# Kernel optimization log

Measured on AMD Instinct MI355X. Metric: run time of the kernel, lower is better.

The kernel has to match this reference:

```python
import jax, jax.numpy as jnp
import numpy as np

M1 = M2 = M3 = 8  # truncated Hartley modes (min(modes, in_channels) in original)


def dht(x):
    # Discrete Hartley transform via 3D FFT over spatial axes: real - imag
    r = jnp.fft.fftn(x, axes=(2, 3, 4))
    return r.real - r.imag


def _mul(a, w):
    # 'bixyz,ioxyz->boxyz' mode-wise channel mixing
    return jnp.einsum('bixyz,ioxyz->boxyz', a, w)


def setup_inputs() -> dict:
    key = jax.random.key(0)
    ks = jax.random.split(key, 5)
    B, Ci, Co = 2, 64, 64
    S1 = S2 = S3 = 64
    scale = 1.0 / (Ci * Co)
    x = jax.random.normal(ks[0], (B, Ci, S1, S2, S3), dtype=jnp.float32)
    wshape = (Ci, Co, M1, M2, M3)
    w1 = scale * jax.random.uniform(ks[1], wshape, dtype=jnp.float32)
    w2 = scale * jax.random.uniform(ks[2], wshape, dtype=jnp.float32)
    w3 = scale * jax.random.uniform(ks[3], wshape, dtype=jnp.float32)
    w4 = scale * jax.random.uniform(ks[4], wshape, dtype=jnp.float32)
    return {"x": x, "w1": w1, "w2": w2, "w3": w3, "w4": w4}


def reference(x, w1, w2, w3, w4):
    b, ci, s1, s2, s3 = x.shape
    co = w1.shape[1]
    # Hartley transform of x ("cos part") and of fully flipped x ("sin part")
    xh = dht(x)
    xhf = dht(x[:, :, ::-1, ::-1, ::-1])

    out_ht = jnp.zeros((b, co, s1, s2, s3), dtype=x.dtype)
    out_ht = out_ht.at[:, :, :M1, :M2, :M3].set(_mul(xh[:, :, :M1, :M2, :M3], w1))
    out_ht = out_ht.at[:, :, -M1:, :M2, :M3].set(_mul(xh[:, :, -M1:, :M2, :M3], w2))
    out_ht = out_ht.at[:, :, :M1, -M2:, :M3].set(_mul(xh[:, :, :M1, -M2:, :M3], w3))
    out_ht = out_ht.at[:, :, -M1:, -M2:, :M3].set(_mul(xh[:, :, -M1:, -M2:, :M3], w4))
    # original zeroes out_ht[:, :, M1:, M2:, M3:] — already zero here since 2*modes <= size

    # inverse DHT = DHT / (D*M*N)
    x_rec = dht(out_ht) / (s1 * s2 * s3)

    # phase = angle(complex(cos_part, sin_part)) = atan2(sin, cos), only on corner block; 0 elsewhere
    phase_corner = jnp.arctan2(xhf[:, :, :M1, :M2, :M3], xh[:, :, :M1, :M2, :M3])
    cos_phase = jnp.ones((b, ci, s1, s2, s3), dtype=x.dtype)
    cos_phase = cos_phase.at[:, :, :M1, :M2, :M3].set(jnp.cos(phase_corner))
    return x_rec * cos_phase
```

## Files before the change

### kernel.cpp

```cpp
#include <hip/hip_runtime.h>
#include <math.h>

struct cf2 { float x, y; };
struct TW64 { float c[64], s[64]; };
struct CF2T { cf2 v[64]; };

constexpr double PI_D = 3.14159265358979323846264338327950288;

constexpr double tsin(double x){
  double x2 = x*x, r = x, t = x;
  t *= -x2/6.0;   r += t;
  t *= -x2/20.0;  r += t;
  t *= -x2/42.0;  r += t;
  t *= -x2/72.0;  r += t;
  t *= -x2/110.0; r += t;
  t *= -x2/156.0; r += t;
  t *= -x2/210.0; r += t;
  t *= -x2/272.0; r += t;
  return r;
}
constexpr double tcos(double x){
  double x2 = x*x, r = 1.0, t = 1.0;
  t *= -x2/2.0;   r += t;
  t *= -x2/12.0;  r += t;
  t *= -x2/30.0;  r += t;
  t *= -x2/56.0;  r += t;
  t *= -x2/90.0;  r += t;
  t *= -x2/132.0; r += t;
  t *= -x2/182.0; r += t;
  t *= -x2/240.0; r += t;
  return r;
}
constexpr double ang_cos(int j){
  int r = j & 15, q = (j >> 4) & 3;
  double a = PI_D/32.0 * r;
  double cc = tcos(a), ss = tsin(a);
  return q==0 ? cc : q==1 ? -ss : q==2 ? -cc : ss;
}
constexpr double ang_sin(int j){
  int r = j & 15, q = (j >> 4) & 3;
  double a = PI_D/32.0 * r;
  double cc = tcos(a), ss = tsin(a);
  return q==0 ? ss : q==1 ? cc : q==2 ? -ss : -cc;
}
constexpr TW64 make_tw(){
  TW64 t{};
  for (int j=0;j<64;j++){ t.c[j] = (float)ang_cos(j); t.s[j] = (float)ang_sin(j); }
  return t;
}
constexpr CF2T make_twi(){
  CF2T r{};
  for (int j=0;j<64;j++){ r.v[j].x = (float)ang_cos(j); r.v[j].y = (float)ang_sin(j); }
  return r;
}
constexpr CF2T make_pq(){
  CF2T r{};
  for (int j=0;j<64;j++){
    double c = ang_cos(j), s = ang_sin(j);
    r.v[j].x = (float)((c + s) / 262144.0);
    r.v[j].y = (float)((s - c) / 262144.0);
  }
  return r;
}

constexpr TW64 TWct = make_tw();
__constant__ CF2T TWIdev = make_twi();
__constant__ CF2T PQdev  = make_pq();

__global__ __launch_bounds__(256) void k_fwd(const float* __restrict__ x, float2* __restrict__ y2g){
  __shared__ float2 y1[8][4][65];
  __shared__ cf2 twl[64];
  int bid = blockIdx.x;
  int n1g = bid & 15, ci_b = bid >> 4;
  int t = threadIdx.x;
  if (t < 64) twl[t] = TWIdev.v[t];
  int n1l = t >> 6, n2 = t & 63;
  int n1 = n1g*4 + n1l;
  const float4* xrow = (const float4*)(x + (((size_t)(ci_b*64 + n1))*64 + n2)*64);
  float xr[64];
  #pragma unroll
  for (int i=0;i<16;i++){
    float4 v = xrow[i];
    xr[4*i]=v.x; xr[4*i+1]=v.y; xr[4*i+2]=v.z; xr[4*i+3]=v.w;
  }
  float yr[8], yi[8];
  #pragma unroll
  for (int k=0;k<8;k++){ yr[k]=0.f; yi[k]=0.f; }
  #pragma unroll
  for (int n3=0;n3<64;n3++){
    float xv = xr[n3];
    #pragma unroll
    for (int k=0;k<8;k++){
      yr[k] = fmaf(xv,  TWct.c[(k*n3)&63], yr[k]);
      yi[k] = fmaf(xv, -TWct.s[(k*n3)&63], yi[k]);
    }
  }
  #pragma unroll
  for (int k=0;k<8;k++) y1[k][n1l][n2] = make_float2(yr[k], yi[k]);
  __syncthreads();
  int w = t >> 6, lane = t & 63;
  int n1c = lane >> 4, k3c = (lane >> 1) & 7, half = lane & 1;
  #pragma unroll
  for (int kk=0;kk<4;kk++){
    int k2i = w*4 + kk;
    int k2 = k2i < 8 ? k2i : 48 + k2i;
    int idx = (k2 * (half*32)) & 63;
    float ar = 0.f, ai = 0.f;
    #pragma unroll 8
    for (int i=0;i<32;i++){
      cf2 tw = twl[idx];
      idx = (idx + k2) & 63;
      float2 y = y1[k3c][n1c][half*32 + i];
      ar = fmaf(y.x, tw.x, fmaf(y.y, tw.y, ar));
      ai = fmaf(y.y, tw.x, fmaf(-y.x, tw.y, ai));
    }
    ar += __shfl_xor(ar, 1, 64);
    ai += __shfl_xor(ai, 1, 64);
    if (half == 0){
      int n1w = n1g*4 + n1c;
      y2g[((size_t)(ci_b*64 + n1w)*16 + k2i)*8 + k3c] = make_float2(ar, ai);
    }
  }
}

template<int K1B>
__device__ __forceinline__ void k2_body(const float2 (*yl)[128], int kk, float* ar, float* ai){
  for (int n1=0;n1<64;n1++){
    float2 y = yl[n1][kk];
    #pragma unroll
    for (int j=0;j<8;j++){
      int k1i = K1B + 2*j;
      int k1 = k1i < 8 ? k1i : 48 + k1i;
      cf2 tw = TWIdev.v[(k1*n1)&63];
      ar[j] = fmaf(y.x, tw.x, fmaf(y.y, tw.y, ar[j]));
      ai[j] = fmaf(y.y, tw.x, fmaf(-y.x, tw.y, ai[j]));
    }
  }
}

__global__ __launch_bounds__(256) void k_fwd_n1(const float2* __restrict__ y2g,
                                                float* __restrict__ xh, float* __restrict__ cp){
  __shared__ float2 yl[64][128];
  int bc = blockIdx.x;
  int t = threadIdx.x;
  const float2* src = y2g + (size_t)bc * 8192;
  #pragma unroll
  for (int j=0;j<32;j++){
    int idx = t + j*256;
    yl[idx>>7][idx&127] = src[idx];
  }
  __syncthreads();
  int kk = t & 127;
  int k2i = kk >> 3, k3 = kk & 7;
  float ar[8], ai[8];
  #pragma unroll
  for (int j=0;j<8;j++){ ar[j]=0.f; ai[j]=0.f; }
  if (t < 128) k2_body<0>(yl, kk, ar, ai);
  else         k2_body<1>(yl, kk, ar, ai);
  int k1base = t >> 7;
  size_t xbase = (size_t)bc * 2048;
  #pragma unroll
  for (int j=0;j<8;j++){
    int k1i = k1base + 2*j;
    float vr = ar[j], vi = ai[j];
    float vxh = vr - vi;
    xh[xbase + k1i*128 + kk] = vxh;
    if (k1i < 8 && k2i < 8){
      int phi = (k1i + k2i + k3) & 63;
      cf2 tw = TWIdev.v[phi];
      float vxhf = vr*(tw.x - tw.y) + vi*(tw.x + tw.y);
      cp[(size_t)bc*512 + k1i*64 + k2i*8 + k3] = cosf(atan2f(vxhf, vxh));
    }
  }
}

__global__ __launch_bounds__(256) void k_mix(const float* __restrict__ xh,
    const float* __restrict__ w1, const float* __restrict__ w2,
    const float* __restrict__ w3, const float* __restrict__ w4,
    float* __restrict__ mh){
  __shared__ float xs[2][64][64];
  __shared__ float wsh[64][64];
  __shared__ float ps[2][128];
  int bid = blockIdx.x;
  int k1l = bid & 7, co = (bid >> 3) & 63, blk = bid >> 9;
  const float* w = (blk==0) ? w1 : (blk==1) ? w2 : (blk==2) ? w3 : w4;
  int k1i = k1l + ((blk & 1) << 3);
  int k2off = (blk & 2) ? 64 : 0;
  int t = threadIdx.x;
  #pragma unroll
  for (int j=0;j<16;j++){
    int idx = t + j*256;
    int ci = idx >> 6, kk = idx & 63;
    wsh[ci][kk] = w[(size_t)(ci*64 + co)*512 + k1l*64 + kk];
  }
  #pragma unroll
  for (int j=0;j<32;j++){
    int idx = t + j*256;
    int b = idx >> 12, ci = (idx >> 6) & 63, kk = idx & 63;
    xs[b][ci][kk] = xh[(size_t)((b*64 + ci)*16 + k1i)*128 + k2off + kk];
  }
  __syncthreads();
  int half = t >> 7, o = t & 127, b = o >> 6, kk = o & 63;
  float acc = 0.f;
  #pragma unroll 8
  for (int i=0;i<32;i++){
    int ci = half*32 + i;
    acc = fmaf(xs[b][ci][kk], wsh[ci][kk], acc);
  }
  ps[half][o] = acc;
  __syncthreads();
  if (t < 128){
    int b2 = t >> 6, kk2 = t & 63;
    mh[(size_t)((b2*64 + co)*16 + k1i)*128 + k2off + kk2] = ps[0][t] + ps[1][t];
  }
}

__global__ __launch_bounds__(256) void k_inv(const float* __restrict__ mh,
                                             const float* __restrict__ cp,
                                             float* __restrict__ out){
  __shared__ float ml[2048];
  __shared__ float2 z1[16][8];
  __shared__ float2 z2[64][8];
  __shared__ cf2 twl[64];
  __shared__ cf2 pql[64];
  int bid = blockIdx.x;
  int n1 = bid & 63, bc = bid >> 6;
  int t = threadIdx.x;
  if (t < 64){ twl[t] = TWIdev.v[t]; pql[t] = PQdev.v[t]; }
  const float* src = mh + (size_t)bc * 2048;
  #pragma unroll
  for (int j=0;j<8;j++) ml[t + j*256] = src[t + j*256];
  __syncthreads();
  if (t < 128){
    float zr = 0.f, zi = 0.f;
    #pragma unroll
    for (int k1i=0;k1i<16;k1i++){
      int k1 = k1i < 8 ? k1i : 48 + k1i;
      cf2 tw = TWIdev.v[(k1*n1)&63];
      float m = ml[k1i*128 + t];
      zr = fmaf(m, tw.x, zr);
      zi = fmaf(m, -tw.y, zi);
    }
    z1[t>>3][t&7] = make_float2(zr, zi);
  }
  __syncthreads();
  #pragma unroll
  for (int jo=0;jo<2;jo++){
    int o = t + jo*256;
    int n2 = o >> 3, k3 = o & 7;
    float zr = 0.f, zi = 0.f;
    #pragma unroll
    for (int k2i=0;k2i<16;k2i++){
      int k2 = k2i < 8 ? k2i : 48 + k2i;
      cf2 tw = twl[(k2*n2)&63];
      float2 z = z1[k2i][k3];
      zr = fmaf(z.x, tw.x, fmaf(z.y, tw.y, zr));
      zi = fmaf(z.y, tw.x, fmaf(-z.x, tw.y, zi));
    }
    z2[n2][k3] = make_float2(zr, zi);
  }
  __syncthreads();
  int n3 = t & 63;
  int n2base = (t >> 6) * 16;
  float p[8], q[8];
  #pragma unroll
  for (int k3=0;k3<8;k3++){
    cf2 pq = pql[(k3*n3)&63];
    p[k3] = pq.x; q[k3] = pq.y;
  }
  float* orow = out + ((size_t)bc*64 + n1)*4096;
  bool corner = (n1 < 8) && (n3 < 8);
  const float* cpr = cp + (size_t)bc*512 + n1*64 + n3;
  #pragma unroll
  for (int j=0;j<16;j++){
    int n2 = n2base + j;
    float v = 0.f;
    #pragma unroll
    for (int k3=0;k3<8;k3++){
      float2 z = z2[n2][k3];
      v = fmaf(z.x, p[k3], fmaf(z.y, q[k3], v));
    }
    if (corner && n2 < 8) v *= cpr[n2*8];
    orow[n2*64 + n3] = v;
  }
}

extern "C" void kernel_launch(void* const* d_in, const int* in_sizes, int n_in,
                              void* d_out, int out_size, void* d_ws, size_t ws_size,
                              hipStream_t stream) {
  (void)in_sizes; (void)n_in; (void)out_size; (void)ws_size;
  const float* x  = (const float*)d_in[0];
  const float* w1 = (const float*)d_in[1];
  const float* w2 = (const float*)d_in[2];
  const float* w3 = (const float*)d_in[3];
  const float* w4 = (const float*)d_in[4];
  float* out = (float*)d_out;
  char* ws = (char*)d_ws;
  float2* y2g = (float2*)ws;
  float*  xh  = (float*)(ws + (8u<<20));
  float*  cp  = (float*)(ws + (9u<<20));
  float*  mh  = (float*)(ws + (9u<<20) + (256u<<10));

  k_fwd   <<<2048, 256, 0, stream>>>(x, y2g);
  k_fwd_n1<<< 128, 256, 0, stream>>>(y2g, xh, cp);
  k_mix   <<<2048, 256, 0, stream>>>(xh, w1, w2, w3, w4, mh);
  k_inv   <<<8192, 256, 0, stream>>>(mh, cp, out);
}
```

Before: 308.1 us.

## Stage x slab through LDS and split forward n3 DFT across threads

The first forward kernel now handles one (ci_b, n1) slab per block. It loads the 64x64 slab coalesced into padded shared memory, where before each thread read a full 256-byte row with strided float4 loads. Each thread then computes only two of the eight n3 frequencies for one row, cutting per-thread register arrays and work, and the grid grows fourfold. The aim is better global coalescing and occupancy, at the cost of redundant row reads from LDS and more blocks.

```diff
diff --git a/kernel.cpp b/kernel.cpp
--- a/kernel.cpp
+++ b/kernel.cpp
@@ -67,58 +67,72 @@
 __constant__ CF2T TWIdev = make_twi();
 __constant__ CF2T PQdev  = make_pq();
 
+
+template<int G>
+__device__ __forceinline__ void stageA(const float* __restrict__ row,
+                                       float& r0, float& i0, float& r1, float& i1){
+  r0=0.f; i0=0.f; r1=0.f; i1=0.f;
+  #pragma unroll
+  for (int n3=0;n3<64;n3++){
+    float xv = row[n3];
+    r0 = fmaf(xv,  TWct.c[((2*G  )*n3)&63], r0);
+    i0 = fmaf(xv, -TWct.s[((2*G  )*n3)&63], i0);
+    r1 = fmaf(xv,  TWct.c[((2*G+1)*n3)&63], r1);
+    i1 = fmaf(xv, -TWct.s[((2*G+1)*n3)&63], i1);
+  }
+}
+
 __global__ __launch_bounds__(256) void k_fwd(const float* __restrict__ x, float2* __restrict__ y2g){
-  __shared__ float2 y1[8][4][65];
+  __shared__ float xt[64*65];
+  __shared__ float2 y1[8*66];
   __shared__ cf2 twl[64];
   int bid = blockIdx.x;
-  int n1g = bid & 15, ci_b = bid >> 4;
+  int n1 = bid & 63, ci_b = bid >> 6;
   int t = threadIdx.x;
   if (t < 64) twl[t] = TWIdev.v[t];
-  int n1l = t >> 6, n2 = t & 63;
-  int n1 = n1g*4 + n1l;
-  const float4* xrow = (const float4*)(x + (((size_t)(ci_b*64 + n1))*64 + n2)*64);
-  float xr[64];
-  #pragma unroll
-  for (int i=0;i<16;i++){
-    float4 v = xrow[i];
-    xr[4*i]=v.x; xr[4*i+1]=v.y; xr[4*i+2]=v.z; xr[4*i+3]=v.w;
-  }
-  float yr[8], yi[8];
-  #pragma unroll
-  for (int k=0;k<8;k++){ yr[k]=0.f; yi[k]=0.f; }
-  #pragma unroll
-  for (int n3=0;n3<64;n3++){
-    float xv = xr[n3];
-    #pragma unroll
-    for (int k=0;k<8;k++){
-      yr[k] = fmaf(xv,  TWct.c[(k*n3)&63], yr[k]);
-      yi[k] = fmaf(xv, -TWct.s[(k*n3)&63], yi[k]);
-    }
-  }
-  #pragma unroll
-  for (int k=0;k<8;k++) y1[k][n1l][n2] = make_float2(yr[k], yi[k]);
-  __syncthreads();
-  int w = t >> 6, lane = t & 63;
-  int n1c = lane >> 4, k3c = (lane >> 1) & 7, half = lane & 1;
-  #pragma unroll
-  for (int kk=0;kk<4;kk++){
-    int k2i = w*4 + kk;
+
+  const float4* src = (const float4*)(x + (size_t)(ci_b*64 + n1)*4096);
+  #pragma unroll
+  for (int j=0;j<4;j++){
+    int q = t + j*256;
+    float4 v = src[q];
+    int n2 = q >> 4, n3 = (q & 15)*4;
+    float* d = &xt[n2*65 + n3];
+    d[0]=v.x; d[1]=v.y; d[2]=v.z; d[3]=v.w;
+  }
+  __syncthreads();
+
+  {
+    int n2 = t & 63, g = t >> 6;
+    const float* row = &xt[n2*65];
+    float r0,i0,r1,i1;
+    if      (g==0) stageA<0>(row,r0,i0,r1,i1);
+    else if (g==1) stageA<1>(row,r0,i0,r1,i1);
+    else if (g==2) stageA<2>(row,r0,i0,r1,i1);
+    else           stageA<3>(row,r0,i0,r1,i1);
+    y1[(2*g  )*66 + n2] = make_float2(r0,i0);
+    y1[(2*g+1)*66 + n2] = make_float2(r1,i1);
+  }
+  __syncthreads();
+
+  {
+    int half = t & 1, k3 = (t >> 1) & 7, k2i = t >> 4;
     int k2 = k2i < 8 ? k2i : 48 + k2i;
     int idx = (k2 * (half*32)) & 63;
+    const float2* yrow = &y1[k3*66 + half*32];
     float ar = 0.f, ai = 0.f;
     #pragma unroll 8
     for (int i=0;i<32;i++){
       cf2 tw = twl[idx];
       idx = (idx + k2) & 63;
-      float2 y = y1[k3c][n1c][half*32 + i];
+      float2 y = yrow[i];
       ar = fmaf(y.x, tw.x, fmaf(y.y, tw.y, ar));
       ai = fmaf(y.y, tw.x, fmaf(-y.x, tw.y, ai));
     }
     ar += __shfl_xor(ar, 1, 64);
     ai += __shfl_xor(ai, 1, 64);
     if (half == 0){
-      int n1w = n1g*4 + n1c;
-      y2g[((size_t)(ci_b*64 + n1w)*16 + k2i)*8 + k3c] = make_float2(ar, ai);
+      y2g[((size_t)(ci_b*64 + n1)*16 + k2i)*8 + k3] = make_float2(ar, ai);
     }
   }
 }
@@ -301,7 +315,7 @@
   float*  cp  = (float*)(ws + (9u<<20));
   float*  mh  = (float*)(ws + (9u<<20) + (256u<<10));
 
-  k_fwd   <<<2048, 256, 0, stream>>>(x, y2g);
+  k_fwd   <<<8192, 256, 0, stream>>>(x, y2g);
   k_fwd_n1<<< 128, 256, 0, stream>>>(y2g, xh, cp);
   k_mix   <<<2048, 256, 0, stream>>>(xh, w1, w2, w3, w4, mh);
   k_inv   <<<8192, 256, 0, stream>>>(mh, cp, out);
```

Measured after the change: 296.7 us. 3.7% less time.
